# Performance work log

Measured on AMD Instinct MI355X. Metric: run time of the kernel, lower is better.

Reference implementation:

```python
import jax, jax.numpy as jnp
import numpy as np

IN_F, HID, OUT_F, N_HEADS, BATCH = 256, 512, 2048, 8, 4096


def _kaiming_uniform(key, shape, fan_in):
    # kaiming_uniform_ with a=sqrt(5): gain = sqrt(2/(1+5)) = 1/sqrt(3)
    gain = 1.0 / np.sqrt(3.0)
    bound = gain * np.sqrt(3.0 / fan_in)  # = sqrt(1/fan_in)
    return jax.random.uniform(key, shape, jnp.float32, -bound, bound)


def setup_inputs() -> dict:
    key = jax.random.key(0)
    kx, ki, k1, k2, k3, k4 = jax.random.split(key, 6)
    X = jax.random.normal(kx, (BATCH, IN_F), jnp.float32)
    X_head_idx = jax.random.randint(ki, (BATCH,), 0, N_HEADS)
    # layer 1: in -> hidden
    W1 = _kaiming_uniform(k1, (N_HEADS, IN_F, HID), IN_F)
    b1 = jax.random.uniform(k2, (N_HEADS, HID), jnp.float32,
                            -1.0 / np.sqrt(IN_F), 1.0 / np.sqrt(IN_F))
    # layer 2: hidden -> out
    W2 = _kaiming_uniform(k3, (N_HEADS, HID, OUT_F), HID)
    b2 = jax.random.uniform(k4, (N_HEADS, OUT_F), jnp.float32,
                            -1.0 / np.sqrt(HID), 1.0 / np.sqrt(HID))
    return {"X": X, "X_head_idx": X_head_idx, "W1": W1, "b1": b1,
            "W2": W2, "b2": b2}


def _selective_linear(x, idx, W, b):
    # x: [B, in], W: [H, in, out], b: [H, out], idx: [B]
    # compute all heads densely, then select each sample's head
    y = jnp.einsum('bi,hio->bho', x, W) + b[None]   # [B, H, out]
    return jnp.take_along_axis(y, idx[:, None, None], axis=1)[:, 0, :]


def reference(X, X_head_idx, W1, b1, W2, b2):
    h = _selective_linear(X, X_head_idx, W1, b1)
    h = jax.nn.relu(h)
    out = _selective_linear(h, X_head_idx, W2, b2)
    return out
```

## Files before the change

### kernel.cpp

```cpp
#include <hip/hip_runtime.h>

#define IN_F 256
#define HID 512
#define OUT_F 2048
#define N_HEADS 8
#define BATCH 4096

typedef __bf16 bf16_t;
typedef bf16_t bf16x8 __attribute__((ext_vector_type(8)));
typedef float f32x4 __attribute__((ext_vector_type(4)));

__device__ inline unsigned short f2bf(float f) {
  union { float f; unsigned u; } v; v.f = f;
  unsigned u = v.u;
  unsigned r = (u + 0x7FFFu + ((u >> 16) & 1u)) >> 16;
  return (unsigned short)r;
}

__global__ __launch_bounds__(1024) void bucket_kernel(const int* __restrict__ idx,
                                                      int* __restrict__ order,
                                                      int* __restrict__ offsets) {
  __shared__ int cnt[N_HEADS];
  __shared__ int base[N_HEADS + 1];
  __shared__ int cur[N_HEADS];
  int tid = threadIdx.x;
  if (tid < N_HEADS) cnt[tid] = 0;
  __syncthreads();
  for (int i = tid; i < BATCH; i += 1024) atomicAdd(&cnt[idx[i]], 1);
  __syncthreads();
  if (tid == 0) {
    int acc = 0;
    for (int h = 0; h < N_HEADS; ++h) { base[h] = acc; cur[h] = acc; acc += cnt[h]; }
    base[N_HEADS] = acc;
  }
  __syncthreads();
  if (tid < N_HEADS + 1) offsets[tid] = base[tid];
  for (int i = tid; i < BATCH; i += 1024) {
    int pos = atomicAdd(&cur[idx[i]], 1);
    order[pos] = i;
  }
}

__global__ __launch_bounds__(256) void gather_x_kernel(const float* __restrict__ X,
                                                       const int* __restrict__ order,
                                                       unsigned short* __restrict__ Xg) {
  int p = blockIdx.x;
  int r = order[p];
  Xg[(size_t)p * IN_F + threadIdx.x] = f2bf(X[(size_t)r * IN_F + threadIdx.x]);
}

__global__ __launch_bounds__(256) void transpose_kernel(const float* __restrict__ W,
                                                        unsigned short* __restrict__ Wt,
                                                        int K, int N) {
  __shared__ float tile[32][33];
  int h = blockIdx.z;
  int n0 = blockIdx.x * 32;
  int k0 = blockIdx.y * 32;
  const float* Wh = W + (size_t)h * K * N;
  unsigned short* Wth = Wt + (size_t)h * K * N;
  int c = threadIdx.x & 31;
  int r = threadIdx.x >> 5;
  for (int rr = r; rr < 32; rr += 8)
    tile[rr][c] = Wh[(size_t)(k0 + rr) * N + n0 + c];
  __syncthreads();
  for (int rr = r; rr < 32; rr += 8)
    Wth[(size_t)(n0 + rr) * K + k0 + c] = f2bf(tile[c][rr]);
}

template <int K, int NTOT, int EPI>
__global__ __launch_bounds__(256) void gemm_kernel(const unsigned short* __restrict__ A,
                                                   const unsigned short* __restrict__ Wt,
                                                   const float* __restrict__ bias,
                                                   const int* __restrict__ offsets,
                                                   const int* __restrict__ order,
                                                   unsigned short* __restrict__ Hout,
                                                   float* __restrict__ Out) {
  constexpr int BM = 64, BN = 64, BK = 32;
  __shared__ __align__(16) unsigned short As[BM * BK];
  __shared__ __align__(16) unsigned short Bs[BN * BK];

  int my = blockIdx.y;
  int off[N_HEADS + 1];
#pragma unroll
  for (int i = 0; i <= N_HEADS; ++i) off[i] = offsets[i];
  int head = -1, row0 = 0, rows = 0, acc_t = 0;
#pragma unroll
  for (int h = 0; h < N_HEADS; ++h) {
    int cnt = off[h + 1] - off[h];
    int t = (cnt + BM - 1) / BM;
    if (head < 0 && my < acc_t + t) {
      head = h;
      int lt = my - acc_t;
      row0 = off[h] + lt * BM;
      rows = min(BM, cnt - lt * BM);
    }
    acc_t += t;
  }
  if (head < 0) return;

  int n0 = blockIdx.x * BN;
  const unsigned short* Bh = Wt + (size_t)head * NTOT * K;

  int tid = threadIdx.x;
  int wave = tid >> 6;
  int lane = tid & 63;
  int q = lane >> 4;
  int l16 = lane & 15;

  f32x4 acc[4];
#pragma unroll
  for (int i = 0; i < 4; ++i) acc[i] = (f32x4){0.f, 0.f, 0.f, 0.f};

  int srow = tid >> 2;
  int scol = (tid & 3) * 8;

  for (int k0 = 0; k0 < K; k0 += BK) {
    uint4 av = make_uint4(0, 0, 0, 0);
    if (srow < rows)
      av = *(const uint4*)(A + (size_t)(row0 + srow) * K + k0 + scol);
    uint4 bv = *(const uint4*)(Bh + (size_t)(n0 + srow) * K + k0 + scol);
    __syncthreads();
    *(uint4*)(As + srow * BK + scol) = av;
    *(uint4*)(Bs + srow * BK + scol) = bv;
    __syncthreads();

    bf16x8 af = *(const bf16x8*)(As + (wave * 16 + l16) * BK + q * 8);
#pragma unroll
    for (int nc = 0; nc < 4; ++nc) {
      bf16x8 bfr = *(const bf16x8*)(Bs + (nc * 16 + l16) * BK + q * 8);
      acc[nc] = __builtin_amdgcn_mfma_f32_16x16x32_bf16(af, bfr, acc[nc], 0, 0, 0);
    }
  }

#pragma unroll
  for (int nc = 0; nc < 4; ++nc) {
    int n = n0 + nc * 16 + l16;
    float bval = bias[(size_t)head * NTOT + n];
#pragma unroll
    for (int r = 0; r < 4; ++r) {
      int m = wave * 16 + q * 4 + r;
      if (m < rows) {
        int p = row0 + m;
        float v = acc[nc][r] + bval;
        if (EPI == 0) {
          v = v > 0.f ? v : 0.f;
          Hout[(size_t)p * NTOT + n] = f2bf(v);
        } else {
          int rg = order[p];
          Out[(size_t)rg * NTOT + n] = v;
        }
      }
    }
  }
}

extern "C" void kernel_launch(void* const* d_in, const int* in_sizes, int n_in,
                              void* d_out, int out_size, void* d_ws, size_t ws_size,
                              hipStream_t stream) {
  const float* X = (const float*)d_in[0];
  const int* idxh = (const int*)d_in[1];
  const float* W1 = (const float*)d_in[2];
  const float* b1 = (const float*)d_in[3];
  const float* W2 = (const float*)d_in[4];
  const float* b2 = (const float*)d_in[5];
  float* out = (float*)d_out;

  char* ws = (char*)d_ws;
  int* order = (int*)ws;                    ws += (size_t)BATCH * 4;
  int* offsets = (int*)ws;                  ws += 64;
  unsigned short* Xg = (unsigned short*)ws; ws += (size_t)BATCH * IN_F * 2;
  unsigned short* W1t = (unsigned short*)ws; ws += (size_t)N_HEADS * IN_F * HID * 2;
  unsigned short* W2t = (unsigned short*)ws; ws += (size_t)N_HEADS * HID * OUT_F * 2;
  unsigned short* Hb = (unsigned short*)ws;  ws += (size_t)BATCH * HID * 2;

  bucket_kernel<<<dim3(1), dim3(1024), 0, stream>>>(idxh, order, offsets);
  transpose_kernel<<<dim3(HID / 32, IN_F / 32, N_HEADS), dim3(256), 0, stream>>>(W1, W1t, IN_F, HID);
  transpose_kernel<<<dim3(OUT_F / 32, HID / 32, N_HEADS), dim3(256), 0, stream>>>(W2, W2t, HID, OUT_F);
  gather_x_kernel<<<dim3(BATCH), dim3(256), 0, stream>>>(X, order, Xg);

  constexpr int MT = BATCH / 64 + N_HEADS;
  gemm_kernel<IN_F, HID, 0><<<dim3(HID / 64, MT), dim3(256), 0, stream>>>(
      Xg, W1t, b1, offsets, order, Hb, nullptr);
  gemm_kernel<HID, OUT_F, 1><<<dim3(OUT_F / 64, MT), dim3(256), 0, stream>>>(
      Hb, W2t, b2, offsets, order, nullptr, out);
}
```

Measured before the change: 149.0 us.

## Enlarge GEMM tiles to 128x128 and load tiles directly into LDS

Rewrites the grouped GEMM to use 128x128 block tiles, with each wave computing a 64x64 sub-tile as a 4x4 grid of MFMAs. Global-to-shared copies now use global_load_lds, bypassing registers. The aim is more data reuse per LDS fragment and fewer load instructions. In exchange it uses more accumulator registers and gives a coarser grid with fewer blocks, which may cut occupancy and waste more work on partial head tiles.

```diff
diff --git a/kernel.cpp b/kernel.cpp
--- a/kernel.cpp
+++ b/kernel.cpp
@@ -9,6 +9,9 @@
 typedef __bf16 bf16_t;
 typedef bf16_t bf16x8 __attribute__((ext_vector_type(8)));
 typedef float f32x4 __attribute__((ext_vector_type(4)));
+
+typedef __attribute__((address_space(1))) const unsigned int gu32;
+typedef __attribute__((address_space(3))) unsigned int lu32;
 
 __device__ inline unsigned short f2bf(float f) {
   union { float f; unsigned u; } v; v.f = f;
@@ -68,30 +71,28 @@
 }
 
 template <int K, int NTOT, int EPI>
-__global__ __launch_bounds__(256) void gemm_kernel(const unsigned short* __restrict__ A,
-                                                   const unsigned short* __restrict__ Wt,
-                                                   const float* __restrict__ bias,
-                                                   const int* __restrict__ offsets,
-                                                   const int* __restrict__ order,
-                                                   unsigned short* __restrict__ Hout,
-                                                   float* __restrict__ Out) {
-  constexpr int BM = 64, BN = 64, BK = 32;
+__global__ __launch_bounds__(256) void gemm128_kernel(const unsigned short* __restrict__ A,
+                                                      const unsigned short* __restrict__ Wt,
+                                                      const float* __restrict__ bias,
+                                                      const int* __restrict__ offsets,
+                                                      const int* __restrict__ order,
+                                                      unsigned short* __restrict__ Hout,
+                                                      float* __restrict__ Out) {
+  constexpr int BM = 128, BN = 128, BK = 32;
   __shared__ __align__(16) unsigned short As[BM * BK];
   __shared__ __align__(16) unsigned short Bs[BN * BK];
 
   int my = blockIdx.y;
-  int off[N_HEADS + 1];
-#pragma unroll
-  for (int i = 0; i <= N_HEADS; ++i) off[i] = offsets[i];
   int head = -1, row0 = 0, rows = 0, acc_t = 0;
 #pragma unroll
   for (int h = 0; h < N_HEADS; ++h) {
-    int cnt = off[h + 1] - off[h];
+    int o0 = offsets[h], o1 = offsets[h + 1];
+    int cnt = o1 - o0;
     int t = (cnt + BM - 1) / BM;
     if (head < 0 && my < acc_t + t) {
       head = h;
       int lt = my - acc_t;
-      row0 = off[h] + lt * BM;
+      row0 = o0 + lt * BM;
       rows = min(BM, cnt - lt * BM);
     }
     acc_t += t;
@@ -99,7 +100,7 @@
   if (head < 0) return;
 
   int n0 = blockIdx.x * BN;
-  const unsigned short* Bh = Wt + (size_t)head * NTOT * K;
+  const unsigned short* Bh = Wt + (size_t)head * (size_t)NTOT * K;
 
   int tid = threadIdx.x;
   int wave = tid >> 6;
@@ -107,47 +108,77 @@
   int q = lane >> 4;
   int l16 = lane & 15;
 
-  f32x4 acc[4];
-#pragma unroll
-  for (int i = 0; i < 4; ++i) acc[i] = (f32x4){0.f, 0.f, 0.f, 0.f};
-
-  int srow = tid >> 2;
-  int scol = (tid & 3) * 8;
+  int ldrow = lane >> 2;
+  int ldcol = (lane & 3) * 8;
+  int c0 = wave * 2, c1 = wave * 2 + 1;
+  int ar0 = row0 + min(c0 * 16 + ldrow, rows - 1);
+  int ar1 = row0 + min(c1 * 16 + ldrow, rows - 1);
+  const unsigned short* aptr0 = A + (size_t)ar0 * K + ldcol;
+  const unsigned short* aptr1 = A + (size_t)ar1 * K + ldcol;
+  const unsigned short* bptr0 = Bh + (size_t)(n0 + c0 * 16 + ldrow) * K + ldcol;
+  const unsigned short* bptr1 = Bh + (size_t)(n0 + c1 * 16 + ldrow) * K + ldcol;
+  unsigned short* lA0 = As + c0 * 512;
+  unsigned short* lA1 = As + c1 * 512;
+  unsigned short* lB0 = Bs + c0 * 512;
+  unsigned short* lB1 = Bs + c1 * 512;
+
+  int w_m = wave >> 1, w_n = wave & 1;
+
+  f32x4 acc[4][4];
+#pragma unroll
+  for (int i = 0; i < 4; ++i)
+#pragma unroll
+    for (int j = 0; j < 4; ++j) acc[i][j] = (f32x4){0.f, 0.f, 0.f, 0.f};
 
   for (int k0 = 0; k0 < K; k0 += BK) {
-    uint4 av = make_uint4(0, 0, 0, 0);
-    if (srow < rows)
-      av = *(const uint4*)(A + (size_t)(row0 + srow) * K + k0 + scol);
-    uint4 bv = *(const uint4*)(Bh + (size_t)(n0 + srow) * K + k0 + scol);
+    __builtin_amdgcn_global_load_lds((gu32*)aptr0, (lu32*)lA0, 16, 0, 0);
+    __builtin_amdgcn_global_load_lds((gu32*)aptr1, (lu32*)lA1, 16, 0, 0);
+    __builtin_amdgcn_global_load_lds((gu32*)bptr0, (lu32*)lB0, 16, 0, 0);
+    __builtin_amdgcn_global_load_lds((gu32*)bptr1, (lu32*)lB1, 16, 0, 0);
+    aptr0 += BK; aptr1 += BK; bptr0 += BK; bptr1 += BK;
     __syncthreads();
-    *(uint4*)(As + srow * BK + scol) = av;
-    *(uint4*)(Bs + srow * BK + scol) = bv;
+
+    bf16x8 af[4], bfr[4];
+#pragma unroll
+    for (int i = 0; i < 4; ++i) {
+      af[i] = *(const bf16x8*)(As + (w_m * 64 + i * 16 + l16) * BK + q * 8);
+      bfr[i] = *(const bf16x8*)(Bs + (w_n * 64 + i * 16 + l16) * BK + q * 8);
+    }
+#pragma unroll
+    for (int mi = 0; mi < 4; ++mi)
+#pragma unroll
+      for (int ni = 0; ni < 4; ++ni)
+        acc[mi][ni] = __builtin_amdgcn_mfma_f32_16x16x32_bf16(af[mi], bfr[ni], acc[mi][ni], 0, 0, 0);
     __syncthreads();
-
-    bf16x8 af = *(const bf16x8*)(As + (wave * 16 + l16) * BK + q * 8);
-#pragma unroll
-    for (int nc = 0; nc < 4; ++nc) {
-      bf16x8 bfr = *(const bf16x8*)(Bs + (nc * 16 + l16) * BK + q * 8);
-      acc[nc] = __builtin_amdgcn_mfma_f32_16x16x32_bf16(af, bfr, acc[nc], 0, 0, 0);
-    }
-  }
-
-#pragma unroll
-  for (int nc = 0; nc < 4; ++nc) {
-    int n = n0 + nc * 16 + l16;
-    float bval = bias[(size_t)head * NTOT + n];
+  }
+
+  float bval[4];
+#pragma unroll
+  for (int ni = 0; ni < 4; ++ni)
+    bval[ni] = bias[(size_t)head * NTOT + n0 + w_n * 64 + ni * 16 + l16];
+
+#pragma unroll
+  for (int mi = 0; mi < 4; ++mi) {
 #pragma unroll
     for (int r = 0; r < 4; ++r) {
-      int m = wave * 16 + q * 4 + r;
+      int m = w_m * 64 + mi * 16 + q * 4 + r;
       if (m < rows) {
         int p = row0 + m;
-        float v = acc[nc][r] + bval;
         if (EPI == 0) {
-          v = v > 0.f ? v : 0.f;
-          Hout[(size_t)p * NTOT + n] = f2bf(v);
+#pragma unroll
+          for (int ni = 0; ni < 4; ++ni) {
+            int n = n0 + w_n * 64 + ni * 16 + l16;
+            float v = acc[mi][ni][r] + bval[ni];
+            v = v > 0.f ? v : 0.f;
+            Hout[(size_t)p * NTOT + n] = f2bf(v);
+          }
         } else {
           int rg = order[p];
-          Out[(size_t)rg * NTOT + n] = v;
+#pragma unroll
+          for (int ni = 0; ni < 4; ++ni) {
+            int n = n0 + w_n * 64 + ni * 16 + l16;
+            Out[(size_t)rg * NTOT + n] = acc[mi][ni][r] + bval[ni];
+          }
         }
       }
     }
@@ -166,9 +197,9 @@
   float* out = (float*)d_out;
 
   char* ws = (char*)d_ws;
-  int* order = (int*)ws;                    ws += (size_t)BATCH * 4;
-  int* offsets = (int*)ws;                  ws += 64;
-  unsigned short* Xg = (unsigned short*)ws; ws += (size_t)BATCH * IN_F * 2;
+  int* order = (int*)ws;                     ws += (size_t)BATCH * 4;
+  int* offsets = (int*)ws;                   ws += 64;
+  unsigned short* Xg = (unsigned short*)ws;  ws += (size_t)BATCH * IN_F * 2;
   unsigned short* W1t = (unsigned short*)ws; ws += (size_t)N_HEADS * IN_F * HID * 2;
   unsigned short* W2t = (unsigned short*)ws; ws += (size_t)N_HEADS * HID * OUT_F * 2;
   unsigned short* Hb = (unsigned short*)ws;  ws += (size_t)BATCH * HID * 2;
@@ -178,9 +209,9 @@
   transpose_kernel<<<dim3(OUT_F / 32, HID / 32, N_HEADS), dim3(256), 0, stream>>>(W2, W2t, HID, OUT_F);
   gather_x_kernel<<<dim3(BATCH), dim3(256), 0, stream>>>(X, order, Xg);
 
-  constexpr int MT = BATCH / 64 + N_HEADS;
-  gemm_kernel<IN_F, HID, 0><<<dim3(HID / 64, MT), dim3(256), 0, stream>>>(
+  constexpr int MT = BATCH / 128 + N_HEADS;
+  gemm128_kernel<IN_F, HID, 0><<<dim3(HID / 128, MT), dim3(256), 0, stream>>>(
       Xg, W1t, b1, offsets, order, Hb, nullptr);
-  gemm_kernel<HID, OUT_F, 1><<<dim3(OUT_F / 64, MT), dim3(256), 0, stream>>>(
+  gemm128_kernel<HID, OUT_F, 1><<<dim3(OUT_F / 128, MT), dim3(256), 0, stream>>>(
       Hb, W2t, b2, offsets, order, nullptr, out);
 }
```

Result: faster. 142.0 us (-4.7%).
